# Kernel optimization log

Hardware: AMD Instinct MI355X
Metric: run time of the kernel (lower is better)

The kernel has to match this reference:

```python
import jax, jax.numpy as jnp
import numpy as np

B, S, D, H = 2, 2048, 1024, 16
HD = D // H  # head_dim = 64


def setup_inputs() -> dict:
    key = jax.random.key(0)
    k1, k2, k3, k4, k5 = jax.random.split(key, 5)
    x = jax.random.normal(k1, (B, S, D), dtype=jnp.float32)
    # causal additive mask [S, S]: 0 on/below diagonal, -1e9 above
    mask = jnp.where(jnp.tril(jnp.ones((S, S), dtype=bool)), 0.0, -1e9).astype(jnp.float32)
    scale = 1.0 / np.sqrt(D)
    W_qkv = jax.random.normal(k2, (D, 3 * D), dtype=jnp.float32) * scale
    b_qkv = jax.random.normal(k3, (3 * D,), dtype=jnp.float32) * 0.01
    W_o = jax.random.normal(k4, (D, D), dtype=jnp.float32) * scale
    b_o = jax.random.normal(k5, (D,), dtype=jnp.float32) * 0.01
    return {"x": x, "mask": mask, "W_qkv": W_qkv, "b_qkv": b_qkv, "W_o": W_o, "b_o": b_o}


def reference(x, mask, W_qkv, b_qkv, W_o, b_o):
    b, s, d = x.shape
    qkv = x @ W_qkv + b_qkv                         # [B,S,3D]
    qkv = qkv.reshape(b, s, H, 3 * HD).transpose(0, 2, 1, 3)  # [B,H,S,3*HD]
    q, k, v = jnp.split(qkv, 3, axis=-1)            # each [B,H,S,HD]
    scores = jnp.einsum('bhqd,bhkd->bhqk', q, k) / np.sqrt(HD)  # [B,H,S,S]
    scores = scores + mask                           # broadcast [S,S] additive mask
    attn = jax.nn.softmax(scores, axis=-1)
    vals = jnp.einsum('bhqk,bhkd->bhqd', attn, v)    # [B,H,S,HD]
    vals = vals.transpose(0, 2, 1, 3).reshape(b, s, d)
    return vals @ W_o + b_o
```

## Files before the change

kernel.cpp:

```cpp
#include <hip/hip_runtime.h>

#define NB 2
#define NS 2048
#define ND 1024
#define NH 16
#define NHD 64
#define QLD (3 * ND)
#define PADP 72
#define PADV 68

typedef unsigned short u16;
typedef __attribute__((ext_vector_type(8))) short short8;
typedef __attribute__((ext_vector_type(4))) short short4v;
typedef __attribute__((ext_vector_type(4))) float f32x4;

__device__ __forceinline__ u16 f2b(float f) {
    unsigned int x = __float_as_uint(f);
    return (u16)((x + 0x7fffu + ((x >> 16) & 1u)) >> 16);
}

__device__ __forceinline__ unsigned int cvtpk(float lo, float hi) {
    unsigned int r;
    asm("v_cvt_pk_bf16_f32 %0, %1, %2" : "=v"(r) : "v"(lo), "v"(hi));
    return r;
}

__global__ __launch_bounds__(256) void convert_bf16(
    const float* __restrict__ src, u16* __restrict__ dst, int n)
{
    const int i = (blockIdx.x * 256 + threadIdx.x) * 8;
    if (i >= n) return;
    float4 a = *(const float4*)(src + i);
    float4 b = *(const float4*)(src + i + 4);
    *(ushort4*)(dst + i)     = make_ushort4(f2b(a.x), f2b(a.y), f2b(a.z), f2b(a.w));
    *(ushort4*)(dst + i + 4) = make_ushort4(f2b(b.x), f2b(b.y), f2b(b.z), f2b(b.w));
}

__global__ __launch_bounds__(256) void transpose_bf16(
    const float* __restrict__ W, u16* __restrict__ WT, int K, int N)
{
    __shared__ u16 Ts[64 * 72];
    const int t = threadIdx.x;
    const int k0 = blockIdx.y << 6, n0 = blockIdx.x << 6;
    const int r = t >> 4, c = (t & 15) << 2;
    #pragma unroll
    for (int rr = 0; rr < 64; rr += 16) {
        float4 v = *(const float4*)&W[(size_t)(k0 + r + rr) * N + n0 + c];
        Ts[(c + 0) * 72 + r + rr] = f2b(v.x);
        Ts[(c + 1) * 72 + r + rr] = f2b(v.y);
        Ts[(c + 2) * 72 + r + rr] = f2b(v.z);
        Ts[(c + 3) * 72 + r + rr] = f2b(v.w);
    }
    __syncthreads();
    const int n = t >> 2, cc = (t & 3) << 4;
    uint4 a = *(const uint4*)&Ts[n * 72 + cc];
    uint4 b = *(const uint4*)&Ts[n * 72 + cc + 8];
    *(uint4*)&WT[(size_t)(n0 + n) * K + k0 + cc]     = a;
    *(uint4*)&WT[(size_t)(n0 + n) * K + k0 + cc + 8] = b;
}

template <int BN, bool STORE_BF16>
__global__ __launch_bounds__(256) void gemm_mfma(
    const u16* __restrict__ A, const u16* __restrict__ BT,
    const float* __restrict__ bias,
    void* __restrict__ C, int M, int N, int K)
{
    constexpr int BIS = BN / 64;
    constexpr int NJ  = BN / 32;
    __shared__ u16 As[128 * 32];
    __shared__ u16 Bs[BN * 32];

    const int tid = threadIdx.x;
    const int wave = tid >> 6, lane = tid & 63;
    const int col = lane & 15, quad = lane >> 4;
    const int wm = wave >> 1, wn = wave & 1;
    const int row0 = blockIdx.y << 7, col0 = blockIdx.x * BN;

    f32x4 acc[4][NJ] = {};

    const u16* asrc[2];
    u16* adst[2];
    #pragma unroll
    for (int is = 0; is < 2; ++is) {
        const int J = is * 256 + wave * 64 + lane;
        const int m = J >> 2;
        const int q = (J & 3) ^ ((m >> 1) & 3);
        asrc[is] = A + (size_t)(row0 + m) * K + q * 8;
        adst[is] = &As[(size_t)(is * 256 + wave * 64) * 8];
    }
    const u16* bsrc[BIS];
    u16* bdst[BIS];
    #pragma unroll
    for (int is = 0; is < BIS; ++is) {
        const int J = is * 256 + wave * 64 + lane;
        const int m = J >> 2;
        const int q = (J & 3) ^ ((m >> 1) & 3);
        bsrc[is] = BT + (size_t)(col0 + m) * K + q * 8;
        bdst[is] = &Bs[(size_t)(is * 256 + wave * 64) * 8];
    }

    for (int kk = 0; kk < K; kk += 32) {
        __syncthreads();
        #pragma unroll
        for (int is = 0; is < 2; ++is)
            __builtin_amdgcn_global_load_lds(
                (const __attribute__((address_space(1))) unsigned int*)(asrc[is] + kk),
                (__attribute__((address_space(3))) unsigned int*)adst[is], 16, 0, 0);
        #pragma unroll
        for (int is = 0; is < BIS; ++is)
            __builtin_amdgcn_global_load_lds(
                (const __attribute__((address_space(1))) unsigned int*)(bsrc[is] + kk),
                (__attribute__((address_space(3))) unsigned int*)bdst[is], 16, 0, 0);
        __syncthreads();

        short8 af[4], bf[NJ];
        #pragma unroll
        for (int i = 0; i < 4; ++i) {
            const int m = wm * 64 + i * 16 + col;
            af[i] = *(const short8*)&As[(m * 4 + (quad ^ ((m >> 1) & 3))) * 8];
        }
        #pragma unroll
        for (int j = 0; j < NJ; ++j) {
            const int n = wn * (BN / 2) + j * 16 + col;
            bf[j] = *(const short8*)&Bs[(n * 4 + (quad ^ ((n >> 1) & 3))) * 8];
        }
        #pragma unroll
        for (int i = 0; i < 4; ++i)
            #pragma unroll
            for (int j = 0; j < NJ; ++j)
                acc[i][j] = __builtin_amdgcn_mfma_f32_16x16x32_bf16(
                    af[i], bf[j], acc[i][j], 0, 0, 0);
    }

    #pragma unroll
    for (int j = 0; j < NJ; ++j) {
        const int gc = col0 + wn * (BN / 2) + j * 16 + col;
        const float bj = bias[gc];
        #pragma unroll
        for (int i = 0; i < 4; ++i) {
            const int gr = row0 + wm * 64 + i * 16 + quad * 4;
            #pragma unroll
            for (int r = 0; r < 4; ++r) {
                const float v = acc[i][j][r] + bj;
                if (STORE_BF16)
                    ((u16*)C)[(size_t)(gr + r) * N + gc] = f2b(v);
                else
                    ((float*)C)[(size_t)(gr + r) * N + gc] = v;
            }
        }
    }
}

__global__ __launch_bounds__(256) void attn_kernel(
    const u16* __restrict__ qkv, u16* __restrict__ vals)
{
    __shared__ u16 Ks[2][64 * 64];
    __shared__ u16 Vt[2][64 * PADV];
    __shared__ u16 Ps[2][64 * PADP];

    const int tid = threadIdx.x;
    const int wave = tid >> 6, lane = tid & 63;
    const int col = lane & 15, quad = lane >> 4;
    const int qtA = blockIdx.x;
    const int qtB = 31 - qtA;
    const int bh = blockIdx.y;
    const int b = bh >> 4, h = bh & 15;
    const size_t base = (size_t)b * NS * QLD + (size_t)h * (3 * NHD);
    const int q0 = wave * 16;
    const int qloc = q0 + col;

    int Jrow[2], Jcol[2];
    #pragma unroll
    for (int is = 0; is < 2; ++is) {
        const int J = is * 256 + wave * 64 + lane;
        Jrow[is] = J >> 3;
        Jcol[is] = ((J & 7) ^ (Jrow[is] & 7)) << 3;
    }

    auto stage_tile = [&](int buf, int srow, int coloff) {
        #pragma unroll
        for (int is = 0; is < 2; ++is) {
            __builtin_amdgcn_global_load_lds(
                (const __attribute__((address_space(1))) unsigned int*)
                    (qkv + base + (size_t)(srow + Jrow[is]) * QLD + coloff + Jcol[is]),
                (__attribute__((address_space(3))) unsigned int*)
                    &Ks[buf][(size_t)(is * 256 + wave * 64) * 8], 16, 0, 0);
        }
    };
    auto read_frag = [&](int buf, int row, int half) -> short8 {
        const int blk = row * 8 + ((quad + (half << 2)) ^ (row & 7));
        return *(const short8*)&Ks[buf][blk << 3];
    };

    const int vtx = tid & 15, vty = tid >> 4;
    const int vk0 = vty << 2, vd0 = vtx << 2;
    auto load_vregs = [&](int kt, ushort4* vr) {
        const u16* vsrc = qkv + base + (size_t)(kt * 64 + vk0) * QLD + 2 * NHD + vd0;
        vr[0] = *(const ushort4*)(vsrc);
        vr[1] = *(const ushort4*)(vsrc + QLD);
        vr[2] = *(const ushort4*)(vsrc + 2 * QLD);
        vr[3] = *(const ushort4*)(vsrc + 3 * QLD);
    };
    auto write_vt = [&](int buf, const ushort4* vr) {
        *(ushort4*)&Vt[buf][(vd0 + 0) * PADV + vk0] =
            make_ushort4(vr[0].x, vr[1].x, vr[2].x, vr[3].x);
        *(ushort4*)&Vt[buf][(vd0 + 1) * PADV + vk0] =
            make_ushort4(vr[0].y, vr[1].y, vr[2].y, vr[3].y);
        *(ushort4*)&Vt[buf][(vd0 + 2) * PADV + vk0] =
            make_ushort4(vr[0].z, vr[1].z, vr[2].z, vr[3].z);
        *(ushort4*)&Vt[buf][(vd0 + 3) * PADV + vk0] =
            make_ushort4(vr[0].w, vr[1].w, vr[2].w, vr[3].w);
    };

    stage_tile(0, qtA * 64, 0);
    stage_tile(1, qtB * 64, 0);
    __syncthreads();
    short8 bqA0 = read_frag(0, qloc, 0), bqA1 = read_frag(0, qloc, 1);
    short8 bqB0 = read_frag(1, qloc, 0), bqB1 = read_frag(1, qloc, 1);
    __syncthreads();

    f32x4 accA[4] = {}, accB[4] = {};
    float mA = -1e30f, lA = 0.f, mB = -1e30f, lB = 0.f;

    auto qk = [&](const short8& b0, const short8& b1,
                  short8 (&kb)[4][2], f32x4 (&s)[4]) {
        __builtin_amdgcn_s_setprio(1);
        #pragma unroll
        for (int kg = 0; kg < 4; ++kg) {
            s[kg] = __builtin_amdgcn_mfma_f32_16x16x32_bf16(kb[kg][0], b0, s[kg], 0, 0, 0);
            s[kg] = __builtin_amdgcn_mfma_f32_16x16x32_bf16(kb[kg][1], b1, s[kg], 0, 0, 0);
        }
        __builtin_amdgcn_s_setprio(0);
    };

    auto sm = [&](f32x4 (&s)[4], f32x4 (&accO)[4], float& m, float& l,
                  bool diag, u16* ps) {
        #pragma unroll
        for (int kg = 0; kg < 4; ++kg)
            #pragma unroll
            for (int r = 0; r < 4; ++r) {
                float v = s[kg][r] * 0.125f;
                if (diag && (kg * 16 + quad * 4 + r > qloc)) v = -1e30f;
                s[kg][r] = v;
            }
        float mx = -1e30f;
        #pragma unroll
        for (int kg = 0; kg < 4; ++kg)
            mx = fmaxf(mx, fmaxf(fmaxf(s[kg][0], s[kg][1]), fmaxf(s[kg][2], s[kg][3])));
        mx = fmaxf(mx, __shfl_xor(mx, 16, 64));
        mx = fmaxf(mx, __shfl_xor(mx, 32, 64));
        if (!__all(mx <= m + 8.f)) {
            const float mn = fmaxf(m, mx);
            const float alpha = __expf(m - mn);
            m = mn;
            l *= alpha;
            #pragma unroll
            for (int dg = 0; dg < 4; ++dg)
                #pragma unroll
                for (int r = 0; r < 4; ++r) accO[dg][r] *= alpha;
        }
        float psum = 0.f;
        #pragma unroll
        for (int kg = 0; kg < 4; ++kg) {
            float p0 = __expf(s[kg][0] - m);
            float p1 = __expf(s[kg][1] - m);
            float p2 = __expf(s[kg][2] - m);
            float p3 = __expf(s[kg][3] - m);
            psum += (p0 + p1) + (p2 + p3);
            uint2 w;
            w.x = cvtpk(p0, p1);
            w.y = cvtpk(p2, p3);
            *(uint2*)&ps[qloc * PADP + kg * 16 + quad * 4] = w;
        }
        psum += __shfl_xor(psum, 16, 64);
        psum += __shfl_xor(psum, 32, 64);
        l += psum;
    };

    auto pv = [&](short8 (&vb)[4][2], f32x4 (&accO)[4], const u16* ps) {
        short8 pb0 = *(const short8*)&ps[qloc * PADP + quad * 8];
        short8 pb1 = *(const short8*)&ps[qloc * PADP + 32 + quad * 8];
        __builtin_amdgcn_s_setprio(1);
        #pragma unroll
        for (int dg = 0; dg < 4; ++dg) {
            accO[dg] = __builtin_amdgcn_mfma_f32_16x16x32_bf16(vb[dg][0], pb0, accO[dg], 0, 0, 0);
            accO[dg] = __builtin_amdgcn_mfma_f32_16x16x32_bf16(vb[dg][1], pb1, accO[dg], 0, 0, 0);
        }
        __builtin_amdgcn_s_setprio(0);
    };

    ushort4 vcur[4], vnxt[4];
    stage_tile(0, 0, NHD);
    load_vregs(0, vcur);

    for (int kt = 0; kt <= qtB; ++kt) {
        const int cur = kt & 1, nxt = cur ^ 1;
        __syncthreads();
        write_vt(cur, vcur);
        __syncthreads();
        if (kt < qtB) {
            stage_tile(nxt, (kt + 1) * 64, NHD);
            load_vregs(kt + 1, vnxt);
        }

        short8 kb[4][2], vb[4][2];
        #pragma unroll
        for (int kg = 0; kg < 4; ++kg) {
            kb[kg][0] = read_frag(cur, kg * 16 + col, 0);
            kb[kg][1] = read_frag(cur, kg * 16 + col, 1);
        }
        #pragma unroll
        for (int dg = 0; dg < 4; ++dg) {
            const int n = dg * 16 + col;
            short4v lo0 = *(const short4v*)&Vt[cur][n * PADV + quad * 8];
            short4v hi0 = *(const short4v*)&Vt[cur][n * PADV + quad * 8 + 4];
            short4v lo1 = *(const short4v*)&Vt[cur][n * PADV + 32 + quad * 8];
            short4v hi1 = *(const short4v*)&Vt[cur][n * PADV + 32 + quad * 8 + 4];
            vb[dg][0] = __builtin_shufflevector(lo0, hi0, 0, 1, 2, 3, 4, 5, 6, 7);
            vb[dg][1] = __builtin_shufflevector(lo1, hi1, 0, 1, 2, 3, 4, 5, 6, 7);
        }

        if (kt <= qtA) {
            f32x4 sB[4] = {}, sA[4] = {};
            qk(bqB0, bqB1, kb, sB);
            qk(bqA0, bqA1, kb, sA);
            sm(sB, accB, mB, lB, false, Ps[0]);
            sm(sA, accA, mA, lA, kt == qtA, Ps[1]);
            pv(vb, accB, Ps[0]);
            pv(vb, accA, Ps[1]);
        } else {
            f32x4 sB[4] = {};
            qk(bqB0, bqB1, kb, sB);
            sm(sB, accB, mB, lB, kt == qtB, Ps[0]);
            pv(vb, accB, Ps[0]);
        }

        #pragma unroll
        for (int i = 0; i < 4; ++i) vcur[i] = vnxt[i];
    }

    {
        const float inv = 1.f / lA;
        const size_t rowoff = ((size_t)b * NS + qtA * 64 + qloc) * ND + h * NHD;
        #pragma unroll
        for (int dg = 0; dg < 4; ++dg) {
            uint2 o;
            o.x = cvtpk(accA[dg][0] * inv, accA[dg][1] * inv);
            o.y = cvtpk(accA[dg][2] * inv, accA[dg][3] * inv);
            *(uint2*)(vals + rowoff + dg * 16 + quad * 4) = o;
        }
    }
    {
        const float inv = 1.f / lB;
        const size_t rowoff = ((size_t)b * NS + qtB * 64 + qloc) * ND + h * NHD;
        #pragma unroll
        for (int dg = 0; dg < 4; ++dg) {
            uint2 o;
            o.x = cvtpk(accB[dg][0] * inv, accB[dg][1] * inv);
            o.y = cvtpk(accB[dg][2] * inv, accB[dg][3] * inv);
            *(uint2*)(vals + rowoff + dg * 16 + quad * 4) = o;
        }
    }
}

extern "C" void kernel_launch(void* const* d_in, const int* in_sizes, int n_in,
                              void* d_out, int out_size, void* d_ws, size_t ws_size,
                              hipStream_t stream)
{
    const float* x    = (const float*)d_in[0];
    const float* Wqkv = (const float*)d_in[2];
    const float* bqkv = (const float*)d_in[3];
    const float* Wo   = (const float*)d_in[4];
    const float* bo   = (const float*)d_in[5];
    float* out = (float*)d_out;

    u16* x_bf   = (u16*)d_ws;
    u16* WqkvT  = x_bf   + (size_t)4096 * 1024;
    u16* WoT    = WqkvT  + (size_t)3072 * 1024;
    u16* qkv    = WoT    + (size_t)1024 * 1024;
    u16* vals   = qkv    + (size_t)4096 * 3072;

    const int M = NB * NS;

    convert_bf16<<<dim3(M * ND / (256 * 8)), dim3(256), 0, stream>>>(
        x, x_bf, M * ND);
    transpose_bf16<<<dim3(QLD / 64, ND / 64), dim3(256), 0, stream>>>(
        Wqkv, WqkvT, ND, QLD);
    transpose_bf16<<<dim3(ND / 64, ND / 64), dim3(256), 0, stream>>>(
        Wo, WoT, ND, ND);

    gemm_mfma<128, true><<<dim3(QLD / 128, M / 128), dim3(256), 0, stream>>>(
        x_bf, WqkvT, bqkv, qkv, M, QLD, ND);
    attn_kernel<<<dim3(16, NB * NH), dim3(256), 0, stream>>>(qkv, vals);
    gemm_mfma<64, false><<<dim3(ND / 64, M / 128), dim3(256), 0, stream>>>(
        vals, WoT, bo, out, M, ND, ND);
}
```

Before: 220.0 us.

## Split paired query tiles into one query tile per attention block

```diff
diff --git a/kernel.cpp b/kernel.cpp
--- a/kernel.cpp
+++ b/kernel.cpp
@@ -155,14 +155,13 @@
     const u16* __restrict__ qkv, u16* __restrict__ vals)
 {
     __shared__ u16 Ks[2][64 * 64];
-    __shared__ u16 Vt[2][64 * PADV];
-    __shared__ u16 Ps[2][64 * PADP];
+    __shared__ u16 Vt[64 * PADV];
+    __shared__ u16 Ps[64 * PADP];
 
     const int tid = threadIdx.x;
     const int wave = tid >> 6, lane = tid & 63;
     const int col = lane & 15, quad = lane >> 4;
-    const int qtA = blockIdx.x;
-    const int qtB = 31 - qtA;
+    const int qt = (blockIdx.x + blockIdx.y) & 31;
     const int bh = blockIdx.y;
     const int b = bh >> 4, h = bh & 15;
     const size_t base = (size_t)b * NS * QLD + (size_t)h * (3 * NHD);
@@ -201,40 +200,36 @@
         vr[2] = *(const ushort4*)(vsrc + 2 * QLD);
         vr[3] = *(const ushort4*)(vsrc + 3 * QLD);
     };
-    auto write_vt = [&](int buf, const ushort4* vr) {
-        *(ushort4*)&Vt[buf][(vd0 + 0) * PADV + vk0] =
+    auto write_vt = [&](const ushort4* vr) {
+        *(ushort4*)&Vt[(vd0 + 0) * PADV + vk0] =
             make_ushort4(vr[0].x, vr[1].x, vr[2].x, vr[3].x);
-        *(ushort4*)&Vt[buf][(vd0 + 1) * PADV + vk0] =
+        *(ushort4*)&Vt[(vd0 + 1) * PADV + vk0] =
             make_ushort4(vr[0].y, vr[1].y, vr[2].y, vr[3].y);
-        *(ushort4*)&Vt[buf][(vd0 + 2) * PADV + vk0] =
+        *(ushort4*)&Vt[(vd0 + 2) * PADV + vk0] =
             make_ushort4(vr[0].z, vr[1].z, vr[2].z, vr[3].z);
-        *(ushort4*)&Vt[buf][(vd0 + 3) * PADV + vk0] =
+        *(ushort4*)&Vt[(vd0 + 3) * PADV + vk0] =
             make_ushort4(vr[0].w, vr[1].w, vr[2].w, vr[3].w);
     };
 
-    stage_tile(0, qtA * 64, 0);
-    stage_tile(1, qtB * 64, 0);
+    stage_tile(0, qt * 64, 0);
     __syncthreads();
-    short8 bqA0 = read_frag(0, qloc, 0), bqA1 = read_frag(0, qloc, 1);
-    short8 bqB0 = read_frag(1, qloc, 0), bqB1 = read_frag(1, qloc, 1);
+    short8 bq0 = read_frag(0, qloc, 0), bq1 = read_frag(0, qloc, 1);
     __syncthreads();
 
-    f32x4 accA[4] = {}, accB[4] = {};
-    float mA = -1e30f, lA = 0.f, mB = -1e30f, lB = 0.f;
-
-    auto qk = [&](const short8& b0, const short8& b1,
-                  short8 (&kb)[4][2], f32x4 (&s)[4]) {
+    f32x4 acc[4] = {};
+    float m = -1e30f, l = 0.f;
+
+    auto qk = [&](short8 (&kb)[4][2], f32x4 (&s)[4]) {
         __builtin_amdgcn_s_setprio(1);
         #pragma unroll
         for (int kg = 0; kg < 4; ++kg) {
-            s[kg] = __builtin_amdgcn_mfma_f32_16x16x32_bf16(kb[kg][0], b0, s[kg], 0, 0, 0);
-            s[kg] = __builtin_amdgcn_mfma_f32_16x16x32_bf16(kb[kg][1], b1, s[kg], 0, 0, 0);
+            s[kg] = __builtin_amdgcn_mfma_f32_16x16x32_bf16(kb[kg][0], bq0, s[kg], 0, 0, 0);
+            s[kg] = __builtin_amdgcn_mfma_f32_16x16x32_bf16(kb[kg][1], bq1, s[kg], 0, 0, 0);
         }
         __builtin_amdgcn_s_setprio(0);
     };
 
-    auto sm = [&](f32x4 (&s)[4], f32x4 (&accO)[4], float& m, float& l,
-                  bool diag, u16* ps) {
+    auto sm = [&](f32x4 (&s)[4], bool diag) {
         #pragma unroll
         for (int kg = 0; kg < 4; ++kg)
             #pragma unroll
@@ -257,7 +252,7 @@
             #pragma unroll
             for (int dg = 0; dg < 4; ++dg)
                 #pragma unroll
-                for (int r = 0; r < 4; ++r) accO[dg][r] *= alpha;
+                for (int r = 0; r < 4; ++r) acc[dg][r] *= alpha;
         }
         float psum = 0.f;
         #pragma unroll
@@ -270,21 +265,21 @@
             uint2 w;
             w.x = cvtpk(p0, p1);
             w.y = cvtpk(p2, p3);
-            *(uint2*)&ps[qloc * PADP + kg * 16 + quad * 4] = w;
+            *(uint2*)&Ps[qloc * PADP + kg * 16 + quad * 4] = w;
         }
         psum += __shfl_xor(psum, 16, 64);
         psum += __shfl_xor(psum, 32, 64);
         l += psum;
     };
 
-    auto pv = [&](short8 (&vb)[4][2], f32x4 (&accO)[4], const u16* ps) {
-        short8 pb0 = *(const short8*)&ps[qloc * PADP + quad * 8];
-        short8 pb1 = *(const short8*)&ps[qloc * PADP + 32 + quad * 8];
+    auto pv = [&](short8 (&vb)[4][2]) {
+        short8 pb0 = *(const short8*)&Ps[qloc * PADP + quad * 8];
+        short8 pb1 = *(const short8*)&Ps[qloc * PADP + 32 + quad * 8];
         __builtin_amdgcn_s_setprio(1);
         #pragma unroll
         for (int dg = 0; dg < 4; ++dg) {
-            accO[dg] = __builtin_amdgcn_mfma_f32_16x16x32_bf16(vb[dg][0], pb0, accO[dg], 0, 0, 0);
-            accO[dg] = __builtin_amdgcn_mfma_f32_16x16x32_bf16(vb[dg][1], pb1, accO[dg], 0, 0, 0);
+            acc[dg] = __builtin_amdgcn_mfma_f32_16x16x32_bf16(vb[dg][0], pb0, acc[dg], 0, 0, 0);
+            acc[dg] = __builtin_amdgcn_mfma_f32_16x16x32_bf16(vb[dg][1], pb1, acc[dg], 0, 0, 0);
         }
         __builtin_amdgcn_s_setprio(0);
     };
@@ -293,12 +288,12 @@
     stage_tile(0, 0, NHD);
     load_vregs(0, vcur);
 
-    for (int kt = 0; kt <= qtB; ++kt) {
+    for (int kt = 0; kt <= qt; ++kt) {
         const int cur = kt & 1, nxt = cur ^ 1;
         __syncthreads();
-        write_vt(cur, vcur);
+        write_vt(vcur);
         __syncthreads();
-        if (kt < qtB) {
+        if (kt < qt) {
             stage_tile(nxt, (kt + 1) * 64, NHD);
             load_vregs(kt + 1, vnxt);
         }
@@ -312,52 +307,31 @@
         #pragma unroll
         for (int dg = 0; dg < 4; ++dg) {
             const int n = dg * 16 + col;
-            short4v lo0 = *(const short4v*)&Vt[cur][n * PADV + quad * 8];
-            short4v hi0 = *(const short4v*)&Vt[cur][n * PADV + quad * 8 + 4];
-            short4v lo1 = *(const short4v*)&Vt[cur][n * PADV + 32 + quad * 8];
-            short4v hi1 = *(const short4v*)&Vt[cur][n * PADV + 32 + quad * 8 + 4];
+            short4v lo0 = *(const short4v*)&Vt[n * PADV + quad * 8];
+            short4v hi0 = *(const short4v*)&Vt[n * PADV + quad * 8 + 4];
+            short4v lo1 = *(const short4v*)&Vt[n * PADV + 32 + quad * 8];
+            short4v hi1 = *(const short4v*)&Vt[n * PADV + 32 + quad * 8 + 4];
             vb[dg][0] = __builtin_shufflevector(lo0, hi0, 0, 1, 2, 3, 4, 5, 6, 7);
             vb[dg][1] = __builtin_shufflevector(lo1, hi1, 0, 1, 2, 3, 4, 5, 6, 7);
         }
 
-        if (kt <= qtA) {
-            f32x4 sB[4] = {}, sA[4] = {};
-            qk(bqB0, bqB1, kb, sB);
-            qk(bqA0, bqA1, kb, sA);
-            sm(sB, accB, mB, lB, false, Ps[0]);
-            sm(sA, accA, mA, lA, kt == qtA, Ps[1]);
-            pv(vb, accB, Ps[0]);
-            pv(vb, accA, Ps[1]);
-        } else {
-            f32x4 sB[4] = {};
-            qk(bqB0, bqB1, kb, sB);
-            sm(sB, accB, mB, lB, kt == qtB, Ps[0]);
-            pv(vb, accB, Ps[0]);
-        }
+        f32x4 s[4] = {};
+        qk(kb, s);
+        sm(s, kt == qt);
+        pv(vb);
 
         #pragma unroll
         for (int i = 0; i < 4; ++i) vcur[i] = vnxt[i];
     }
 
     {
-        const float inv = 1.f / lA;
-        const size_t rowoff = ((size_t)b * NS + qtA * 64 + qloc) * ND + h * NHD;
+        const float inv = 1.f / l;
+        const size_t rowoff = ((size_t)b * NS + qt * 64 + qloc) * ND + h * NHD;
         #pragma unroll
         for (int dg = 0; dg < 4; ++dg) {
             uint2 o;
-            o.x = cvtpk(accA[dg][0] * inv, accA[dg][1] * inv);
-            o.y = cvtpk(accA[dg][2] * inv, accA[dg][3] * inv);
-            *(uint2*)(vals + rowoff + dg * 16 + quad * 4) = o;
-        }
-    }
-    {
-        const float inv = 1.f / lB;
-        const size_t rowoff = ((size_t)b * NS + qtB * 64 + qloc) * ND + h * NHD;
-        #pragma unroll
-        for (int dg = 0; dg < 4; ++dg) {
-            uint2 o;
-            o.x = cvtpk(accB[dg][0] * inv, accB[dg][1] * inv);
-            o.y = cvtpk(accB[dg][2] * inv, accB[dg][3] * inv);
+            o.x = cvtpk(acc[dg][0] * inv, acc[dg][1] * inv);
+            o.y = cvtpk(acc[dg][2] * inv, acc[dg][3] * inv);
             *(uint2*)(vals + rowoff + dg * 16 + quad * 4) = o;
         }
     }
@@ -391,7 +365,7 @@
 
     gemm_mfma<128, true><<<dim3(QLD / 128, M / 128), dim3(256), 0, stream>>>(
         x_bf, WqkvT, bqkv, qkv, M, QLD, ND);
-    attn_kernel<<<dim3(16, NB * NH), dim3(256), 0, stream>>>(qkv, vals);
+    attn_kernel<<<dim3(32, NB * NH), dim3(256), 0, stream>>>(qkv, vals);
     gemm_mfma<64, false><<<dim3(ND / 64, M / 128), dim3(256), 0, stream>>>(
         vals, WoT, bo, out, M, ND, ND);
 }
```

Result: slower. 228.7 us (+4.0%).

## Widen attention KV tile to 128 keys and use exp2-based softmax

Applied to the files above, without the earlier changes.

```diff
diff --git a/kernel.cpp b/kernel.cpp
--- a/kernel.cpp
+++ b/kernel.cpp
@@ -6,12 +6,12 @@
 #define NH 16
 #define NHD 64
 #define QLD (3 * ND)
-#define PADP 72
-#define PADV 68
+#define KVB 128
+#define PADP 136
+#define PADV 136
 
 typedef unsigned short u16;
 typedef __attribute__((ext_vector_type(8))) short short8;
-typedef __attribute__((ext_vector_type(4))) short short4v;
 typedef __attribute__((ext_vector_type(4))) float f32x4;
 
 __device__ __forceinline__ u16 f2b(float f) {
@@ -154,9 +154,9 @@
 __global__ __launch_bounds__(256) void attn_kernel(
     const u16* __restrict__ qkv, u16* __restrict__ vals)
 {
-    __shared__ u16 Ks[2][64 * 64];
-    __shared__ u16 Vt[2][64 * PADV];
-    __shared__ u16 Ps[2][64 * PADP];
+    __shared__ u16 Ks[2][KVB * 64];
+    __shared__ u16 Vt[64 * PADV];
+    __shared__ u16 Ps[64 * PADP];
 
     const int tid = threadIdx.x;
     const int wave = tid >> 6, lane = tid & 63;
@@ -166,23 +166,32 @@
     const int bh = blockIdx.y;
     const int b = bh >> 4, h = bh & 15;
     const size_t base = (size_t)b * NS * QLD + (size_t)h * (3 * NHD);
-    const int q0 = wave * 16;
-    const int qloc = q0 + col;
-
-    int Jrow[2], Jcol[2];
+    const int qloc = wave * 16 + col;
+
+    int Jrow[4], Jcol[4];
     #pragma unroll
-    for (int is = 0; is < 2; ++is) {
+    for (int is = 0; is < 4; ++is) {
         const int J = is * 256 + wave * 64 + lane;
         Jrow[is] = J >> 3;
         Jcol[is] = ((J & 7) ^ (Jrow[is] & 7)) << 3;
     }
 
-    auto stage_tile = [&](int buf, int srow, int coloff) {
+    auto stage_k = [&](int buf, int kt) {
+        #pragma unroll
+        for (int is = 0; is < 4; ++is) {
+            __builtin_amdgcn_global_load_lds(
+                (const __attribute__((address_space(1))) unsigned int*)
+                    (qkv + base + (size_t)(kt * KVB + Jrow[is]) * QLD + NHD + Jcol[is]),
+                (__attribute__((address_space(3))) unsigned int*)
+                    &Ks[buf][(size_t)(is * 256 + wave * 64) * 8], 16, 0, 0);
+        }
+    };
+    auto stage_q = [&](int buf, int qt) {
         #pragma unroll
         for (int is = 0; is < 2; ++is) {
             __builtin_amdgcn_global_load_lds(
                 (const __attribute__((address_space(1))) unsigned int*)
-                    (qkv + base + (size_t)(srow + Jrow[is]) * QLD + coloff + Jcol[is]),
+                    (qkv + base + (size_t)(qt * 64 + Jrow[is]) * QLD + Jcol[is]),
                 (__attribute__((address_space(3))) unsigned int*)
                     &Ks[buf][(size_t)(is * 256 + wave * 64) * 8], 16, 0, 0);
         }
@@ -193,27 +202,25 @@
     };
 
     const int vtx = tid & 15, vty = tid >> 4;
-    const int vk0 = vty << 2, vd0 = vtx << 2;
+    const int vk0 = vty << 3, vd0 = vtx << 2;
     auto load_vregs = [&](int kt, ushort4* vr) {
-        const u16* vsrc = qkv + base + (size_t)(kt * 64 + vk0) * QLD + 2 * NHD + vd0;
-        vr[0] = *(const ushort4*)(vsrc);
-        vr[1] = *(const ushort4*)(vsrc + QLD);
-        vr[2] = *(const ushort4*)(vsrc + 2 * QLD);
-        vr[3] = *(const ushort4*)(vsrc + 3 * QLD);
-    };
-    auto write_vt = [&](int buf, const ushort4* vr) {
-        *(ushort4*)&Vt[buf][(vd0 + 0) * PADV + vk0] =
-            make_ushort4(vr[0].x, vr[1].x, vr[2].x, vr[3].x);
-        *(ushort4*)&Vt[buf][(vd0 + 1) * PADV + vk0] =
-            make_ushort4(vr[0].y, vr[1].y, vr[2].y, vr[3].y);
-        *(ushort4*)&Vt[buf][(vd0 + 2) * PADV + vk0] =
-            make_ushort4(vr[0].z, vr[1].z, vr[2].z, vr[3].z);
-        *(ushort4*)&Vt[buf][(vd0 + 3) * PADV + vk0] =
-            make_ushort4(vr[0].w, vr[1].w, vr[2].w, vr[3].w);
-    };
-
-    stage_tile(0, qtA * 64, 0);
-    stage_tile(1, qtB * 64, 0);
+        const u16* vsrc = qkv + base + (size_t)(kt * KVB + vk0) * QLD + 2 * NHD + vd0;
+        #pragma unroll
+        for (int j = 0; j < 8; ++j) vr[j] = *(const ushort4*)(vsrc + j * QLD);
+    };
+    auto write_vt = [&](const ushort4* vr) {
+        *(ushort4*)&Vt[(vd0 + 0) * PADV + vk0]     = make_ushort4(vr[0].x, vr[1].x, vr[2].x, vr[3].x);
+        *(ushort4*)&Vt[(vd0 + 0) * PADV + vk0 + 4] = make_ushort4(vr[4].x, vr[5].x, vr[6].x, vr[7].x);
+        *(ushort4*)&Vt[(vd0 + 1) * PADV + vk0]     = make_ushort4(vr[0].y, vr[1].y, vr[2].y, vr[3].y);
+        *(ushort4*)&Vt[(vd0 + 1) * PADV + vk0 + 4] = make_ushort4(vr[4].y, vr[5].y, vr[6].y, vr[7].y);
+        *(ushort4*)&Vt[(vd0 + 2) * PADV + vk0]     = make_ushort4(vr[0].z, vr[1].z, vr[2].z, vr[3].z);
+        *(ushort4*)&Vt[(vd0 + 2) * PADV + vk0 + 4] = make_ushort4(vr[4].z, vr[5].z, vr[6].z, vr[7].z);
+        *(ushort4*)&Vt[(vd0 + 3) * PADV + vk0]     = make_ushort4(vr[0].w, vr[1].w, vr[2].w, vr[3].w);
+        *(ushort4*)&Vt[(vd0 + 3) * PADV + vk0 + 4] = make_ushort4(vr[4].w, vr[5].w, vr[6].w, vr[7].w);
+    };
+
+    stage_q(0, qtA);
+    stage_q(1, qtB);
     __syncthreads();
     short8 bqA0 = read_frag(0, qloc, 0), bqA1 = read_frag(0, qloc, 1);
     short8 bqB0 = read_frag(1, qloc, 0), bqB1 = read_frag(1, qloc, 1);
@@ -222,121 +229,121 @@
     f32x4 accA[4] = {}, accB[4] = {};
     float mA = -1e30f, lA = 0.f, mB = -1e30f, lB = 0.f;
 
-    auto qk = [&](const short8& b0, const short8& b1,
-                  short8 (&kb)[4][2], f32x4 (&s)[4]) {
+    const float SCL = 0.18033688f;
+    const float DTHR = 11.5416f;
+
+    auto qk = [&](const short8& b0, const short8& b1, int buf, f32x4 (&s)[8]) {
         __builtin_amdgcn_s_setprio(1);
         #pragma unroll
-        for (int kg = 0; kg < 4; ++kg) {
-            s[kg] = __builtin_amdgcn_mfma_f32_16x16x32_bf16(kb[kg][0], b0, s[kg], 0, 0, 0);
-            s[kg] = __builtin_amdgcn_mfma_f32_16x16x32_bf16(kb[kg][1], b1, s[kg], 0, 0, 0);
+        for (int kg = 0; kg < 8; ++kg) {
+            short8 k0 = read_frag(buf, kg * 16 + col, 0);
+            short8 k1 = read_frag(buf, kg * 16 + col, 1);
+            s[kg] = __builtin_amdgcn_mfma_f32_16x16x32_bf16(k0, b0, s[kg], 0, 0, 0);
+            s[kg] = __builtin_amdgcn_mfma_f32_16x16x32_bf16(k1, b1, s[kg], 0, 0, 0);
         }
         __builtin_amdgcn_s_setprio(0);
     };
 
-    auto sm = [&](f32x4 (&s)[4], f32x4 (&accO)[4], float& m, float& l,
-                  bool diag, u16* ps) {
-        #pragma unroll
-        for (int kg = 0; kg < 4; ++kg)
+    auto sm = [&](f32x4 (&s)[8], f32x4 (&acc)[4], float& m, float& l,
+                  bool diag, int thresh) {
+        #pragma unroll
+        for (int kg = 0; kg < 8; ++kg)
             #pragma unroll
             for (int r = 0; r < 4; ++r) {
-                float v = s[kg][r] * 0.125f;
-                if (diag && (kg * 16 + quad * 4 + r > qloc)) v = -1e30f;
+                float v = s[kg][r] * SCL;
+                if (diag && (kg * 16 + quad * 4 + r > thresh)) v = -1e30f;
                 s[kg][r] = v;
             }
         float mx = -1e30f;
         #pragma unroll
-        for (int kg = 0; kg < 4; ++kg)
+        for (int kg = 0; kg < 8; ++kg)
             mx = fmaxf(mx, fmaxf(fmaxf(s[kg][0], s[kg][1]), fmaxf(s[kg][2], s[kg][3])));
         mx = fmaxf(mx, __shfl_xor(mx, 16, 64));
         mx = fmaxf(mx, __shfl_xor(mx, 32, 64));
-        if (!__all(mx <= m + 8.f)) {
+        if (!__all(mx <= m + DTHR)) {
             const float mn = fmaxf(m, mx);
-            const float alpha = __expf(m - mn);
+            const float alpha = exp2f(m - mn);
             m = mn;
             l *= alpha;
             #pragma unroll
             for (int dg = 0; dg < 4; ++dg)
                 #pragma unroll
-                for (int r = 0; r < 4; ++r) accO[dg][r] *= alpha;
+                for (int r = 0; r < 4; ++r) acc[dg][r] *= alpha;
         }
         float psum = 0.f;
         #pragma unroll
-        for (int kg = 0; kg < 4; ++kg) {
-            float p0 = __expf(s[kg][0] - m);
-            float p1 = __expf(s[kg][1] - m);
-            float p2 = __expf(s[kg][2] - m);
-            float p3 = __expf(s[kg][3] - m);
+        for (int kg = 0; kg < 8; ++kg) {
+            float p0 = exp2f(s[kg][0] - m);
+            float p1 = exp2f(s[kg][1] - m);
+            float p2 = exp2f(s[kg][2] - m);
+            float p3 = exp2f(s[kg][3] - m);
             psum += (p0 + p1) + (p2 + p3);
             uint2 w;
             w.x = cvtpk(p0, p1);
             w.y = cvtpk(p2, p3);
-            *(uint2*)&ps[qloc * PADP + kg * 16 + quad * 4] = w;
+            *(uint2*)&Ps[qloc * PADP + kg * 16 + quad * 4] = w;
         }
         psum += __shfl_xor(psum, 16, 64);
         psum += __shfl_xor(psum, 32, 64);
         l += psum;
     };
 
-    auto pv = [&](short8 (&vb)[4][2], f32x4 (&accO)[4], const u16* ps) {
-        short8 pb0 = *(const short8*)&ps[qloc * PADP + quad * 8];
-        short8 pb1 = *(const short8*)&ps[qloc * PADP + 32 + quad * 8];
+    auto pv = [&](const short8 (&vb)[4][4], f32x4 (&acc)[4]) {
+        short8 pb[4];
+        #pragma unroll
+        for (int c = 0; c < 4; ++c)
+            pb[c] = *(const short8*)&Ps[qloc * PADP + c * 32 + quad * 8];
         __builtin_amdgcn_s_setprio(1);
         #pragma unroll
-        for (int dg = 0; dg < 4; ++dg) {
-            accO[dg] = __builtin_amdgcn_mfma_f32_16x16x32_bf16(vb[dg][0], pb0, accO[dg], 0, 0, 0);
-            accO[dg] = __builtin_amdgcn_mfma_f32_16x16x32_bf16(vb[dg][1], pb1, accO[dg], 0, 0, 0);
-        }
+        for (int dg = 0; dg < 4; ++dg)
+            #pragma unroll
+            for (int c = 0; c < 4; ++c)
+                acc[dg] = __builtin_amdgcn_mfma_f32_16x16x32_bf16(
+                    vb[dg][c], pb[c], acc[dg], 0, 0, 0);
         __builtin_amdgcn_s_setprio(0);
     };
 
-    ushort4 vcur[4], vnxt[4];
-    stage_tile(0, 0, NHD);
+    const int qtAh = qtA >> 1, qtBh = qtB >> 1;
+    const int thA = qloc + ((qtA & 1) << 6);
+    const int thB = qloc + ((qtB & 1) << 6);
+    ushort4 vcur[8], vnxt[8];
+    stage_k(0, 0);
     load_vregs(0, vcur);
 
-    for (int kt = 0; kt <= qtB; ++kt) {
+    for (int kt = 0; kt <= qtBh; ++kt) {
         const int cur = kt & 1, nxt = cur ^ 1;
         __syncthreads();
-        write_vt(cur, vcur);
+        write_vt(vcur);
         __syncthreads();
-        if (kt < qtB) {
-            stage_tile(nxt, (kt + 1) * 64, NHD);
+        if (kt < qtBh) {
+            stage_k(nxt, kt + 1);
             load_vregs(kt + 1, vnxt);
         }
 
-        short8 kb[4][2], vb[4][2];
-        #pragma unroll
-        for (int kg = 0; kg < 4; ++kg) {
-            kb[kg][0] = read_frag(cur, kg * 16 + col, 0);
-            kb[kg][1] = read_frag(cur, kg * 16 + col, 1);
-        }
+        short8 vb[4][4];
         #pragma unroll
         for (int dg = 0; dg < 4; ++dg) {
             const int n = dg * 16 + col;
-            short4v lo0 = *(const short4v*)&Vt[cur][n * PADV + quad * 8];
-            short4v hi0 = *(const short4v*)&Vt[cur][n * PADV + quad * 8 + 4];
-            short4v lo1 = *(const short4v*)&Vt[cur][n * PADV + 32 + quad * 8];
-            short4v hi1 = *(const short4v*)&Vt[cur][n * PADV + 32 + quad * 8 + 4];
-            vb[dg][0] = __builtin_shufflevector(lo0, hi0, 0, 1, 2, 3, 4, 5, 6, 7);
-            vb[dg][1] = __builtin_shufflevector(lo1, hi1, 0, 1, 2, 3, 4, 5, 6, 7);
-        }
-
-        if (kt <= qtA) {
-            f32x4 sB[4] = {}, sA[4] = {};
-            qk(bqB0, bqB1, kb, sB);
-            qk(bqA0, bqA1, kb, sA);
-            sm(sB, accB, mB, lB, false, Ps[0]);
-            sm(sA, accA, mA, lA, kt == qtA, Ps[1]);
-            pv(vb, accB, Ps[0]);
-            pv(vb, accA, Ps[1]);
-        } else {
-            f32x4 sB[4] = {};
-            qk(bqB0, bqB1, kb, sB);
-            sm(sB, accB, mB, lB, kt == qtB, Ps[0]);
-            pv(vb, accB, Ps[0]);
-        }
-
-        #pragma unroll
-        for (int i = 0; i < 4; ++i) vcur[i] = vnxt[i];
+            #pragma unroll
+            for (int c = 0; c < 4; ++c)
+                vb[dg][c] = *(const short8*)&Vt[n * PADV + c * 32 + quad * 8];
+        }
+
+        {
+            f32x4 s[8] = {};
+            qk(bqB0, bqB1, cur, s);
+            sm(s, accB, mB, lB, kt == qtBh, thB);
+            pv(vb, accB);
+        }
+        if (kt <= qtAh) {
+            f32x4 s[8] = {};
+            qk(bqA0, bqA1, cur, s);
+            sm(s, accA, mA, lA, kt == qtAh, thA);
+            pv(vb, accA);
+        }
+
+        #pragma unroll
+        for (int i = 0; i < 8; ++i) vcur[i] = vnxt[i];
     }
 
     {
```

Result: slower. 243.3 us (+10.6%).
